# Performance work log

Measured on AMD Instinct MI355X. Metric: run time of the kernel, lower is better.

## Reference

```python
import jax, jax.numpy as jnp
import numpy as np

EPS = 1e-8
STRIDE = 1
PADDING = 1  # init_kwargs padding


def setup_inputs() -> dict:
    key = jax.random.key(0)
    k1, k2, k3, k4 = jax.random.split(key, 4)
    B, IC, OC, DL, K, H, W = 16, 256, 256, 512, 3, 64, 64
    return {
        "image": jax.random.normal(k1, (B, IC, H, W), dtype=jnp.float32),
        "style": jax.random.normal(k2, (B, DL), dtype=jnp.float32),
        "weight": jax.random.normal(k3, (OC, IC, K, K), dtype=jnp.float32),
        "mod_weight": jax.random.normal(k4, (IC, DL), dtype=jnp.float32),
    }


def reference(image, style, weight, mod_weight):
    B, IC, H, W = image.shape
    OC, _, K, _ = weight.shape
    DL = mod_weight.shape[1]

    # WeightScaledLinear: style -> per-input-channel modulation scale s [B, IC]
    mod_scale = np.sqrt(2.0 / DL).astype(np.float32)
    s = style @ (mod_weight * mod_scale).T  # [B, IC]

    # Conv weight equalized-lr scale
    w_scale = np.sqrt(2.0 / (IC * K * K)).astype(np.float32)

    # Demodulation uses the UNSCALED base weight (faithful to source):
    # rsqrt(sum_{ic,kh,kw} weight^2 + eps), per output channel [OC]
    demod = jax.lax.rsqrt(jnp.sum(weight * weight, axis=(1, 2, 3)) + EPS)

    # Per-sample modulated conv == scale input channels by s, then shared conv,
    # then scale output channels by demod. This folds the groups=batch trick
    # into a single batched conv (identical math).
    x = image * s[:, :, None, None]  # [B, IC, H, W]
    out = jax.lax.conv_general_dilated(
        x, weight * w_scale,
        window_strides=(STRIDE, STRIDE),
        padding=[(PADDING, PADDING), (PADDING, PADDING)],
        dimension_numbers=("NCHW", "OIHW", "NCHW"),
    )  # [B, OC, H, W]
    return out * demod[None, :, None, None]
```

## Files before the change

kernel.cpp:

```cpp
#include <hip/hip_runtime.h>

typedef __bf16 bf16x8 __attribute__((ext_vector_type(8)));
typedef float  f32x4  __attribute__((ext_vector_type(4)));

#define IC    256
#define OC    256
#define Hh    64
#define Ww    64
#define Bb    16
#define DLEN  512
#define KKTOT 2304
#define HP    66
#define MODSCALE 0.0625f
#define WSCALE   0.029462782549439484f

#define XT_ELEMS  (Bb*HP*HP*IC)
#define XT_BYTES  (XT_ELEMS*2)
#define WMAT_OFF  XT_BYTES
#define WMAT_BYTES (OC*KKTOT*2)
#define S_OFF     (WMAT_OFF + WMAT_BYTES)

typedef const __attribute__((address_space(1))) unsigned int* gptr_t;
typedef __attribute__((address_space(3))) unsigned int* lptr_t;

__device__ __forceinline__ void gl2lds16(const void* g, void* l) {
  __builtin_amdgcn_global_load_lds((gptr_t)g, (lptr_t)l, 16, 0, 0);
}

__global__ void k_style(const float* __restrict__ style,
                        const float* __restrict__ mw,
                        float* __restrict__ s_out) {
  __shared__ float st[DLEN];
  const int b = blockIdx.x, t = threadIdx.x;
  st[t]       = style[b*DLEN + t];
  st[t + 256] = style[b*DLEN + t + 256];
  __syncthreads();
  const float4* mwr = (const float4*)(mw + (long)t*DLEN);
  float acc = 0.f;
  #pragma unroll 4
  for (int d = 0; d < DLEN/4; ++d) {
    float4 v = mwr[d];
    acc += v.x*st[d*4] + v.y*st[d*4+1] + v.z*st[d*4+2] + v.w*st[d*4+3];
  }
  s_out[b*IC + t] = acc * MODSCALE;
}

__global__ void k_wmat(const float* __restrict__ wt, __bf16* __restrict__ wmat) {
  const int oc = blockIdx.x, t = threadIdx.x;
  float w9[9];
  const float* p = wt + ((long)oc*IC + t)*9;
  float ss = 0.f;
  #pragma unroll
  for (int r = 0; r < 9; ++r) { w9[r] = p[r]; ss += w9[r]*w9[r]; }
  #pragma unroll
  for (int off = 32; off; off >>= 1) ss += __shfl_down(ss, off, 64);
  __shared__ float red[4];
  if ((t & 63) == 0) red[t >> 6] = ss;
  __syncthreads();
  float total = red[0] + red[1] + red[2] + red[3];
  float dm = WSCALE / sqrtf(total + 1e-8f);
  #pragma unroll
  for (int r = 0; r < 9; ++r)
    wmat[oc*KKTOT + r*IC + t] = (__bf16)(w9[r] * dm);
}

__global__ void k_halo(__bf16* __restrict__ xt) {
  const int b = blockIdx.x, t = threadIdx.x;
  uint4* base = (uint4*)(xt + (long)b*HP*HP*IC);
  const uint4 z = {0u,0u,0u,0u};
  for (int i = t; i < 2112; i += 256) { base[i] = z; base[137280 + i] = z; }
  for (int i = t; i < 64*32; i += 256) {
    int y = 1 + (i >> 5), c = i & 31;
    base[y*2112 + c] = z;
    base[y*2112 + 2080 + c] = z;
  }
}

__global__ void k_xmod(const float* __restrict__ img,
                       const float* __restrict__ s,
                       __bf16* __restrict__ xt) {
  __shared__ float tile[64][69];
  const int t   = threadIdx.x;
  const int b   = blockIdx.x >> 8;
  const int rem = blockIdx.x & 255;
  const int y   = rem >> 2;
  const int ic0 = (rem & 3) << 6;
  #pragma unroll
  for (int r = 0; r < 4; ++r) {
    int seg = r*256 + t;
    int i   = seg >> 4;
    int x0  = (seg & 15) * 4;
    float4 v = *(const float4*)(img + (((long)(b*IC + ic0 + i)*Hh + y)*Ww + x0));
    float sv = s[b*IC + ic0 + i];
    tile[i][x0+0] = v.x*sv; tile[i][x0+1] = v.y*sv;
    tile[i][x0+2] = v.z*sv; tile[i][x0+3] = v.w*sv;
  }
  __syncthreads();
  const int x  = t >> 2;
  const int j0 = (t & 3) << 4;
  bf16x8 o0, o1;
  #pragma unroll
  for (int e = 0; e < 8; ++e) o0[e] = (__bf16)tile[j0 + e][x];
  #pragma unroll
  for (int e = 0; e < 8; ++e) o1[e] = (__bf16)tile[j0 + 8 + e][x];
  __bf16* dst = xt + (((long)(b*HP + y + 1)*HP + (x + 1))*IC + ic0 + j0);
  ((bf16x8*)dst)[0] = o0;
  ((bf16x8*)dst)[1] = o1;
}

__global__ __launch_bounds__(512, 2) void k_conv(const __bf16* __restrict__ wmat,
                                                 const __bf16* __restrict__ xt,
                                                 float* __restrict__ out) {
  __shared__ __attribute__((aligned(128))) char ldsc[131072];
  const int tid  = threadIdx.x;
  const int lane = tid & 63;
  const int wv   = tid >> 6;
  const int wr   = wv >> 2;
  const int wc   = wv & 3;

  const int bi     = blockIdx.x;
  const int b      = ((bi & 7) << 1) | ((bi >> 7) & 1);
  const int hwBase = ((bi >> 3) & 15) << 8;

  const int row0 = tid >> 3;
  const int c8   = (tid & 7) ^ (row0 & 7);
  const long aOff0 = (long)row0*KKTOT + c8*8;
  const long aOff1 = aOff0 + (long)64*KKTOT;
  const int x  = row0;
  const int y0 = hwBase >> 6;
  long bOff[2][2];
  #pragma unroll
  for (int h = 0; h < 2; ++h)
    #pragma unroll
    for (int l = 0; l < 2; ++l)
      bOff[h][l] = (((long)b*HP + y0 + 2*h + l)*HP + x)*IC + c8*8;
  const unsigned wvOff = wv << 10;

#define STAGE_A(tt, h) do {                                              \
    char* d_ = ldsc + (((tt)&1)<<16) + ((h)<<14) + wvOff;                \
    const __bf16* g_ = wmat + (h)*(128*KKTOT) + (tt)*64;                 \
    gl2lds16(g_ + aOff0, d_);                                            \
    gl2lds16(g_ + aOff1, d_ + 8192);                                     \
  } while (0)

#define STAGE_B(tt, h, sb) do {                                          \
    char* d_ = ldsc + (((tt)&1)<<16) + 32768 + ((h)<<14) + wvOff;        \
    gl2lds16(xt + bOff[h][0] + (sb), d_);                                \
    gl2lds16(xt + bOff[h][1] + (sb), d_ + 8192);                         \
  } while (0)

  STAGE_A(0, 0); STAGE_A(0, 1);
  STAGE_B(0, 0, 0); STAGE_B(0, 1, 0);
  __syncthreads();

  f32x4 acc[8][4] = {};
  bf16x8 af[2][2];
  bf16x8 bfr[4][2];
  const int cb = (lane >> 4) << 4;
  const int rA = wr*128 + (lane & 15);
  const int rB = wc*64  + (lane & 15);

#define READ_A(q) do {                                                   \
    _Pragma("unroll")                                                    \
    for (int m2 = 0; m2 < 2; ++m2) {                                     \
      int rr = rA + (q)*32 + m2*16, sw = (rr & 7) << 4;                  \
      af[m2][0] = *(const bf16x8*)(Abuf + rr*128 + ((  0 + cb) ^ sw));   \
      af[m2][1] = *(const bf16x8*)(Abuf + rr*128 + (( 64 + cb) ^ sw));   \
    }                                                                    \
  } while (0)

#define MFMA_Q(q) do {                                                   \
    __builtin_amdgcn_s_setprio(1);                                       \
    _Pragma("unroll")                                                    \
    for (int ks = 0; ks < 2; ++ks)                                       \
      _Pragma("unroll")                                                  \
      for (int m2 = 0; m2 < 2; ++m2)                                     \
        _Pragma("unroll")                                                \
        for (int n = 0; n < 4; ++n)                                      \
          acc[(q)*2+m2][n] = __builtin_amdgcn_mfma_f32_16x16x32_bf16(af[m2][ks], bfr[n][ks], acc[(q)*2+m2][n], 0, 0, 0); \
    __builtin_amdgcn_s_setprio(0);                                       \
  } while (0)

  for (int t = 0; t < 36; ++t) {
    char* Abuf = ldsc + ((t & 1) << 16);
    char* Bbuf = Abuf + 32768;
    const int tt = t + 1, pos = tt >> 2, kh = pos/3;
    const int sb1 = (kh*HP + (pos - kh*3))*IC + ((tt & 3) << 6);

    #pragma unroll
    for (int n = 0; n < 4; ++n) {
      int rr = rB + n*16, sw = (rr & 7) << 4;
      bfr[n][0] = *(const bf16x8*)(Bbuf + rr*128 + ((  0 + cb) ^ sw));
      bfr[n][1] = *(const bf16x8*)(Bbuf + rr*128 + (( 64 + cb) ^ sw));
    }
    READ_A(0);
    if (t < 35) { STAGE_A(tt, 0); STAGE_B(tt, 0, sb1); }
    MFMA_Q(0);

    READ_A(1);
    if (t < 35) { STAGE_A(tt, 1); STAGE_B(tt, 1, sb1); }
    MFMA_Q(1);

    READ_A(2);
    MFMA_Q(2);
    READ_A(3);
    MFMA_Q(3);

    __syncthreads();
  }

  float* outb = out + (((long)b*OC + wr*128 + ((lane >> 4) << 2))*(Hh*Ww))
                    + hwBase + wc*64 + (lane & 15);
  #pragma unroll
  for (int m = 0; m < 8; ++m)
    #pragma unroll
    for (int n = 0; n < 4; ++n)
      #pragma unroll
      for (int j = 0; j < 4; ++j)
        outb[((long)(m*16 + j))*(Hh*Ww) + n*16] = acc[m][n][j];
}

extern "C" void kernel_launch(void* const* d_in, const int* in_sizes, int n_in,
                              void* d_out, int out_size, void* d_ws, size_t ws_size,
                              hipStream_t stream) {
  const float* image = (const float*)d_in[0];
  const float* style = (const float*)d_in[1];
  const float* weight= (const float*)d_in[2];
  const float* modw  = (const float*)d_in[3];
  float* out = (float*)d_out;

  char* ws = (char*)d_ws;
  __bf16* xt   = (__bf16*)ws;
  __bf16* wmat = (__bf16*)(ws + WMAT_OFF);
  float*  sbuf = (float*)(ws + S_OFF);

  k_style<<<Bb, 256, 0, stream>>>(style, modw, sbuf);
  k_wmat<<<OC, 256, 0, stream>>>(weight, wmat);
  k_halo<<<Bb, 256, 0, stream>>>(xt);
  k_xmod<<<Bb*64*4, 256, 0, stream>>>(image, sbuf, xt);
  k_conv<<<256, 512, 0, stream>>>(wmat, xt, out);
}
```

Measured before the change: 108.7 us.

## Load conv B operand directly from global into registers, halve LDS

The conv kernel stops staging the image (B) tile through LDS. Each wave now loads its B fragments straight from global memory into registers, double-buffered across K steps, so LDS only holds the weight (A) tiles and shrinks from 128KB to 64KB. The halo-zeroing kernel is folded into k_xmod as extra blocks, saving one launch. This cuts LDS traffic and footprint, which could help occupancy, but it depends on the global and L2 latency of the direct loads being hidden, and it adds register pressure.

```diff
diff --git a/kernel.cpp b/kernel.cpp
--- a/kernel.cpp
+++ b/kernel.cpp
@@ -64,23 +64,23 @@
     wmat[oc*KKTOT + r*IC + t] = (__bf16)(w9[r] * dm);
 }
 
-__global__ void k_halo(__bf16* __restrict__ xt) {
-  const int b = blockIdx.x, t = threadIdx.x;
-  uint4* base = (uint4*)(xt + (long)b*HP*HP*IC);
-  const uint4 z = {0u,0u,0u,0u};
-  for (int i = t; i < 2112; i += 256) { base[i] = z; base[137280 + i] = z; }
-  for (int i = t; i < 64*32; i += 256) {
-    int y = 1 + (i >> 5), c = i & 31;
-    base[y*2112 + c] = z;
-    base[y*2112 + 2080 + c] = z;
-  }
-}
-
 __global__ void k_xmod(const float* __restrict__ img,
                        const float* __restrict__ s,
                        __bf16* __restrict__ xt) {
+  const int t = threadIdx.x;
+  if (blockIdx.x >= Bb*256) {
+    const int b = blockIdx.x - Bb*256;
+    uint4* base = (uint4*)(xt + (long)b*HP*HP*IC);
+    const uint4 z = {0u,0u,0u,0u};
+    for (int i = t; i < 2112; i += 256) { base[i] = z; base[137280 + i] = z; }
+    for (int i = t; i < 64*32; i += 256) {
+      int y = 1 + (i >> 5), c = i & 31;
+      base[y*2112 + c] = z;
+      base[y*2112 + 2080 + c] = z;
+    }
+    return;
+  }
   __shared__ float tile[64][69];
-  const int t   = threadIdx.x;
   const int b   = blockIdx.x >> 8;
   const int rem = blockIdx.x & 255;
   const int y   = rem >> 2;
@@ -111,7 +111,7 @@
 __global__ __launch_bounds__(512, 2) void k_conv(const __bf16* __restrict__ wmat,
                                                  const __bf16* __restrict__ xt,
                                                  float* __restrict__ out) {
-  __shared__ __attribute__((aligned(128))) char ldsc[131072];
+  __shared__ __attribute__((aligned(128))) char ldsc[65536];
   const int tid  = threadIdx.x;
   const int lane = tid & 63;
   const int wv   = tid >> 6;
@@ -126,39 +126,40 @@
   const int c8   = (tid & 7) ^ (row0 & 7);
   const long aOff0 = (long)row0*KKTOT + c8*8;
   const long aOff1 = aOff0 + (long)64*KKTOT;
-  const int x  = row0;
-  const int y0 = hwBase >> 6;
-  long bOff[2][2];
-  #pragma unroll
-  for (int h = 0; h < 2; ++h)
-    #pragma unroll
-    for (int l = 0; l < 2; ++l)
-      bOff[h][l] = (((long)b*HP + y0 + 2*h + l)*HP + x)*IC + c8*8;
   const unsigned wvOff = wv << 10;
 
 #define STAGE_A(tt, h) do {                                              \
-    char* d_ = ldsc + (((tt)&1)<<16) + ((h)<<14) + wvOff;                \
+    char* d_ = ldsc + (((tt)&1)<<15) + ((h)<<14) + wvOff;                \
     const __bf16* g_ = wmat + (h)*(128*KKTOT) + (tt)*64;                 \
     gl2lds16(g_ + aOff0, d_);                                            \
     gl2lds16(g_ + aOff1, d_ + 8192);                                     \
   } while (0)
 
-#define STAGE_B(tt, h, sb) do {                                          \
-    char* d_ = ldsc + (((tt)&1)<<16) + 32768 + ((h)<<14) + wvOff;        \
-    gl2lds16(xt + bOff[h][0] + (sb), d_);                                \
-    gl2lds16(xt + bOff[h][1] + (sb), d_ + 8192);                         \
-  } while (0)
-
-  STAGE_A(0, 0); STAGE_A(0, 1);
-  STAGE_B(0, 0, 0); STAGE_B(0, 1, 0);
-  __syncthreads();
+  const int y0w = (hwBase >> 6) + wc;
+  const int xl  = lane & 15;
+  const int kq  = (lane >> 4) << 3;
+  const __bf16* bb[4];
+  {
+    const __bf16* bb0 = xt + ((long)(b*HP + y0w)*HP)*IC + kq;
+    #pragma unroll
+    for (int n = 0; n < 4; ++n) bb[n] = bb0 + (n*16 + xl)*IC;
+  }
+
+#define LOAD_B(dst, tt) do {                                             \
+    int pos_ = (tt) >> 2, kh_ = pos_ / 3, kw_ = pos_ - kh_*3;            \
+    long so_ = (long)((kh_*HP + kw_)*IC + (((tt) & 3) << 6));            \
+    _Pragma("unroll")                                                    \
+    for (int n = 0; n < 4; ++n) {                                        \
+      dst[n][0] = *(const bf16x8*)(bb[n] + so_);                         \
+      dst[n][1] = *(const bf16x8*)(bb[n] + so_ + 32);                    \
+    }                                                                    \
+  } while (0)
 
   f32x4 acc[8][4] = {};
   bf16x8 af[2][2];
-  bf16x8 bfr[4][2];
+  bf16x8 bfrA[4][2], bfrB[4][2];
   const int cb = (lane >> 4) << 4;
   const int rA = wr*128 + (lane & 15);
-  const int rB = wc*64  + (lane & 15);
 
 #define READ_A(q) do {                                                   \
     _Pragma("unroll")                                                    \
@@ -169,7 +170,7 @@
     }                                                                    \
   } while (0)
 
-#define MFMA_Q(q) do {                                                   \
+#define MFMA_Q(q, BF) do {                                               \
     __builtin_amdgcn_s_setprio(1);                                       \
     _Pragma("unroll")                                                    \
     for (int ks = 0; ks < 2; ++ks)                                       \
@@ -177,36 +178,34 @@
       for (int m2 = 0; m2 < 2; ++m2)                                     \
         _Pragma("unroll")                                                \
         for (int n = 0; n < 4; ++n)                                      \
-          acc[(q)*2+m2][n] = __builtin_amdgcn_mfma_f32_16x16x32_bf16(af[m2][ks], bfr[n][ks], acc[(q)*2+m2][n], 0, 0, 0); \
+          acc[(q)*2+m2][n] = __builtin_amdgcn_mfma_f32_16x16x32_bf16(af[m2][ks], BF[n][ks], acc[(q)*2+m2][n], 0, 0, 0); \
     __builtin_amdgcn_s_setprio(0);                                       \
   } while (0)
 
-  for (int t = 0; t < 36; ++t) {
-    char* Abuf = ldsc + ((t & 1) << 16);
-    char* Bbuf = Abuf + 32768;
-    const int tt = t + 1, pos = tt >> 2, kh = pos/3;
-    const int sb1 = (kh*HP + (pos - kh*3))*IC + ((tt & 3) << 6);
-
-    #pragma unroll
-    for (int n = 0; n < 4; ++n) {
-      int rr = rB + n*16, sw = (rr & 7) << 4;
-      bfr[n][0] = *(const bf16x8*)(Bbuf + rr*128 + ((  0 + cb) ^ sw));
-      bfr[n][1] = *(const bf16x8*)(Bbuf + rr*128 + (( 64 + cb) ^ sw));
-    }
-    READ_A(0);
-    if (t < 35) { STAGE_A(tt, 0); STAGE_B(tt, 0, sb1); }
-    MFMA_Q(0);
-
-    READ_A(1);
-    if (t < 35) { STAGE_A(tt, 1); STAGE_B(tt, 1, sb1); }
-    MFMA_Q(1);
-
-    READ_A(2);
-    MFMA_Q(2);
-    READ_A(3);
-    MFMA_Q(3);
-
-    __syncthreads();
+#define TILE(t_, CUR, NXT, doNext, nt_) do {                             \
+    char* Abuf = ldsc + (((t_) & 1) << 15);                              \
+    READ_A(0);                                                           \
+    if (doNext) LOAD_B(NXT, nt_);                                        \
+    if ((t_) < 35) STAGE_A((t_)+1, 0);                                   \
+    MFMA_Q(0, CUR);                                                      \
+    READ_A(1);                                                           \
+    if ((t_) < 35) STAGE_A((t_)+1, 1);                                   \
+    MFMA_Q(1, CUR);                                                      \
+    READ_A(2);                                                           \
+    MFMA_Q(2, CUR);                                                      \
+    READ_A(3);                                                           \
+    MFMA_Q(3, CUR);                                                      \
+    __syncthreads();                                                     \
+  } while (0)
+
+  LOAD_B(bfrA, 0);
+  STAGE_A(0, 0); STAGE_A(0, 1);
+  __syncthreads();
+
+  for (int tp = 0; tp < 18; ++tp) {
+    const int t0 = tp * 2;
+    TILE(t0,     bfrA, bfrB, 1,         t0 + 1);
+    TILE(t0 + 1, bfrB, bfrA, (tp < 17), t0 + 2);
   }
 
   float* outb = out + (((long)b*OC + wr*128 + ((lane >> 4) << 2))*(Hh*Ww))
@@ -236,7 +235,6 @@
 
   k_style<<<Bb, 256, 0, stream>>>(style, modw, sbuf);
   k_wmat<<<OC, 256, 0, stream>>>(weight, wmat);
-  k_halo<<<Bb, 256, 0, stream>>>(xt);
-  k_xmod<<<Bb*64*4, 256, 0, stream>>>(image, sbuf, xt);
+  k_xmod<<<Bb*256 + Bb, 256, 0, stream>>>(image, sbuf, xt);
   k_conv<<<256, 512, 0, stream>>>(wmat, xt, out);
 }
```

Result: slower. 134.6 us (+23.9%).

## Double-buffer A fragments in conv loop and merge halo zeroing into xmod

Applied to the files above, without the earlier changes.

The conv main loop now keeps two sets of A-fragment registers, so LDS reads for the next quarter are issued before the MFMAs of the current one. This is meant to hide LDS latency behind matrix work, at the cost of more VGPRs under the 512-thread, 2-block launch bound. Separately, the halo-zeroing kernel becomes extra blocks of the xmod kernel, removing one kernel launch.

```diff
diff --git a/kernel.cpp b/kernel.cpp
--- a/kernel.cpp
+++ b/kernel.cpp
@@ -64,23 +64,23 @@
     wmat[oc*KKTOT + r*IC + t] = (__bf16)(w9[r] * dm);
 }
 
-__global__ void k_halo(__bf16* __restrict__ xt) {
-  const int b = blockIdx.x, t = threadIdx.x;
-  uint4* base = (uint4*)(xt + (long)b*HP*HP*IC);
-  const uint4 z = {0u,0u,0u,0u};
-  for (int i = t; i < 2112; i += 256) { base[i] = z; base[137280 + i] = z; }
-  for (int i = t; i < 64*32; i += 256) {
-    int y = 1 + (i >> 5), c = i & 31;
-    base[y*2112 + c] = z;
-    base[y*2112 + 2080 + c] = z;
-  }
-}
-
 __global__ void k_xmod(const float* __restrict__ img,
                        const float* __restrict__ s,
                        __bf16* __restrict__ xt) {
+  const int t = threadIdx.x;
+  if (blockIdx.x >= Bb*256) {
+    const int b = blockIdx.x - Bb*256;
+    uint4* base = (uint4*)(xt + (long)b*HP*HP*IC);
+    const uint4 z = {0u,0u,0u,0u};
+    for (int i = t; i < 2112; i += 256) { base[i] = z; base[137280 + i] = z; }
+    for (int i = t; i < 64*32; i += 256) {
+      int y = 1 + (i >> 5), c = i & 31;
+      base[y*2112 + c] = z;
+      base[y*2112 + 2080 + c] = z;
+    }
+    return;
+  }
   __shared__ float tile[64][69];
-  const int t   = threadIdx.x;
   const int b   = blockIdx.x >> 8;
   const int rem = blockIdx.x & 255;
   const int y   = rem >> 2;
@@ -145,8 +145,8 @@
 
 #define STAGE_B(tt, h, sb) do {                                          \
     char* d_ = ldsc + (((tt)&1)<<16) + 32768 + ((h)<<14) + wvOff;        \
-    gl2lds16(xt + bOff[h][0] + (sb), d_);                                \
-    gl2lds16(xt + bOff[h][1] + (sb), d_ + 8192);                         \
+    gl2lds16(xt + bOff[h][0] + (sb), d_);                                 \
+    gl2lds16(xt + bOff[h][1] + (sb), d_ + 8192);                          \
   } while (0)
 
   STAGE_A(0, 0); STAGE_A(0, 1);
@@ -154,22 +154,22 @@
   __syncthreads();
 
   f32x4 acc[8][4] = {};
-  bf16x8 af[2][2];
+  bf16x8 af0[2][2], af1[2][2];
   bf16x8 bfr[4][2];
   const int cb = (lane >> 4) << 4;
   const int rA = wr*128 + (lane & 15);
   const int rB = wc*64  + (lane & 15);
 
-#define READ_A(q) do {                                                   \
+#define READ_A_TO(AF, q) do {                                            \
     _Pragma("unroll")                                                    \
     for (int m2 = 0; m2 < 2; ++m2) {                                     \
       int rr = rA + (q)*32 + m2*16, sw = (rr & 7) << 4;                  \
-      af[m2][0] = *(const bf16x8*)(Abuf + rr*128 + ((  0 + cb) ^ sw));   \
-      af[m2][1] = *(const bf16x8*)(Abuf + rr*128 + (( 64 + cb) ^ sw));   \
+      AF[m2][0] = *(const bf16x8*)(Abuf + rr*128 + ((  0 + cb) ^ sw));   \
+      AF[m2][1] = *(const bf16x8*)(Abuf + rr*128 + (( 64 + cb) ^ sw));   \
     }                                                                    \
   } while (0)
 
-#define MFMA_Q(q) do {                                                   \
+#define MFMA_Q(q, AF) do {                                               \
     __builtin_amdgcn_s_setprio(1);                                       \
     _Pragma("unroll")                                                    \
     for (int ks = 0; ks < 2; ++ks)                                       \
@@ -177,7 +177,7 @@
       for (int m2 = 0; m2 < 2; ++m2)                                     \
         _Pragma("unroll")                                                \
         for (int n = 0; n < 4; ++n)                                      \
-          acc[(q)*2+m2][n] = __builtin_amdgcn_mfma_f32_16x16x32_bf16(af[m2][ks], bfr[n][ks], acc[(q)*2+m2][n], 0, 0, 0); \
+          acc[(q)*2+m2][n] = __builtin_amdgcn_mfma_f32_16x16x32_bf16(AF[m2][ks], bfr[n][ks], acc[(q)*2+m2][n], 0, 0, 0); \
     __builtin_amdgcn_s_setprio(0);                                       \
   } while (0)
 
@@ -193,18 +193,19 @@
       bfr[n][0] = *(const bf16x8*)(Bbuf + rr*128 + ((  0 + cb) ^ sw));
       bfr[n][1] = *(const bf16x8*)(Bbuf + rr*128 + (( 64 + cb) ^ sw));
     }
-    READ_A(0);
+    READ_A_TO(af0, 0);
+    READ_A_TO(af1, 1);
     if (t < 35) { STAGE_A(tt, 0); STAGE_B(tt, 0, sb1); }
-    MFMA_Q(0);
-
-    READ_A(1);
+
+    MFMA_Q(0, af0);
+    READ_A_TO(af0, 2);
     if (t < 35) { STAGE_A(tt, 1); STAGE_B(tt, 1, sb1); }
-    MFMA_Q(1);
-
-    READ_A(2);
-    MFMA_Q(2);
-    READ_A(3);
-    MFMA_Q(3);
+
+    MFMA_Q(1, af1);
+    READ_A_TO(af1, 3);
+
+    MFMA_Q(2, af0);
+    MFMA_Q(3, af1);
 
     __syncthreads();
   }
@@ -236,7 +237,6 @@
 
   k_style<<<Bb, 256, 0, stream>>>(style, modw, sbuf);
   k_wmat<<<OC, 256, 0, stream>>>(weight, wmat);
-  k_halo<<<Bb, 256, 0, stream>>>(xt);
-  k_xmod<<<Bb*64*4, 256, 0, stream>>>(image, sbuf, xt);
+  k_xmod<<<Bb*256 + Bb, 256, 0, stream>>>(image, sbuf, xt);
   k_conv<<<256, 512, 0, stream>>>(wmat, xt, out);
 }
```

After: 107.0 us. No clear change (-1.6%).
